# Optimization experiments

Hardware: AMD Instinct MI355X
Metric: run time of the kernel (lower is better)

Reference implementation:

```python
import jax, jax.numpy as jnp
import numpy as np

N = 100000
K = 5
ALPHA = 0.1
IN_DIM, HID_DIM, OUT_DIM = 512, 256, 64


def setup_inputs() -> dict:
    key = jax.random.key(0)
    k1, k2, k3, k4, k5, k6 = jax.random.split(key, 6)
    E = 3200000
    x = jax.random.normal(k1, (N, IN_DIM), dtype=jnp.float32)
    edge_index = jax.random.randint(k2, (2, E), 0, N, dtype=jnp.int32)
    s1 = 1.0 / np.sqrt(IN_DIM)
    s2 = 1.0 / np.sqrt(HID_DIM)
    W1 = jax.random.uniform(k3, (IN_DIM, HID_DIM), jnp.float32, -s1, s1)
    b1 = jax.random.uniform(k4, (HID_DIM,), jnp.float32, -s1, s1)
    W2 = jax.random.uniform(k5, (HID_DIM, OUT_DIM), jnp.float32, -s2, s2)
    b2 = jax.random.uniform(k6, (OUT_DIM,), jnp.float32, -s2, s2)
    return {"x": x, "edge_index": edge_index, "W1": W1, "b1": b1, "W2": W2, "b2": b2}


def _gcn_norm(edge_index, num_nodes):
    # add self loops, symmetric normalization D^-1/2 (A+I) D^-1/2
    loop = jnp.arange(num_nodes, dtype=edge_index.dtype)
    row = jnp.concatenate([edge_index[0], loop])
    col = jnp.concatenate([edge_index[1], loop])
    w = jnp.ones(row.shape[0], dtype=jnp.float32)
    deg = jax.ops.segment_sum(w, col, num_segments=num_nodes)
    dinv = jnp.where(deg > 0, jax.lax.rsqrt(deg), 0.0)
    norm = dinv[row] * w * dinv[col]
    return row, col, norm


def reference(x, edge_index, W1, b1, W2, b2):
    # MLP (dropout = identity in eval mode)
    h = jax.nn.relu(x @ W1 + b1) @ W2 + b2  # [N, OUT_DIM]
    row, col, norm = _gcn_norm(edge_index, N)
    x0 = h
    for _ in range(K):
        msg = h[row] * norm[:, None]                    # gather + scale [E+N, OUT_DIM]
        h = jax.ops.segment_sum(msg, col, num_segments=N)  # scatter-add
        h = (1.0 - ALPHA) * h + ALPHA * x0
    return jax.nn.log_softmax(h, axis=1)
```

## Files before the change

### kernel.cpp

```cpp
#include <hip/hip_runtime.h>

#define IN_DIM  512
#define HID_DIM 256
#define OUT_DIM 64
#define KPROP   5
#define ALPHA   0.1f

#define BKT_SHIFT 9
#define PART_EPB  8192

typedef short short8v __attribute__((ext_vector_type(8)));
typedef float f32x4   __attribute__((ext_vector_type(4)));

__device__ __forceinline__ unsigned short f2bf(float f) {
    unsigned u = __builtin_bit_cast(unsigned, f);
    unsigned r = (u + 0x7FFFu + ((u >> 16) & 1u)) >> 16;
    return (unsigned short)r;
}
__device__ __forceinline__ float bflo(unsigned v) { return __builtin_bit_cast(float, v << 16); }
__device__ __forceinline__ float bfhi(unsigned v) { return __builtin_bit_cast(float, v & 0xffff0000u); }

__global__ __launch_bounds__(256) void bucket_count_kernel(const int* __restrict__ ei, int E,
                                                           int* __restrict__ bucketCnt) {
    __shared__ int hist[256];
    int t = threadIdx.x;
    hist[t] = 0;
    __syncthreads();
    int e0 = blockIdx.x * PART_EPB;
#pragma unroll 4
    for (int i = 0; i < PART_EPB / 256; ++i) {
        int e = e0 + i * 256 + t;
        if (e < E) atomicAdd(&hist[ei[E + e] >> BKT_SHIFT], 1);
    }
    __syncthreads();
    if (hist[t] > 0) atomicAdd(&bucketCnt[t], hist[t]);
}

__global__ __launch_bounds__(256) void bucket_scan_kernel(const int* __restrict__ bucketCnt,
                                                          int* __restrict__ bucketBase,
                                                          int* __restrict__ bucketFill,
                                                          int* __restrict__ indptr,
                                                          int E, int N) {
    __shared__ int sm[256];
    int t = threadIdx.x;
    int v = bucketCnt[t];
    sm[t] = v;
    __syncthreads();
    for (int off = 1; off < 256; off <<= 1) {
        int add = 0;
        if (t >= off) add = sm[t - off];
        __syncthreads();
        if (t >= off) sm[t] += add;
        __syncthreads();
    }
    int base = sm[t] - v;
    bucketBase[t] = base;
    bucketFill[t] = base;
    if (t == 0) indptr[N] = E;
}

__global__ __launch_bounds__(256) void partition_kernel(const int* __restrict__ ei, int E,
                                                        int* __restrict__ bucketFill,
                                                        int* __restrict__ packed) {
    __shared__ int hist[256];
    __shared__ int base[256];
    int t = threadIdx.x;
    int e0 = blockIdx.x * PART_EPB;
    hist[t] = 0;
    __syncthreads();
#pragma unroll 4
    for (int i = 0; i < PART_EPB / 256; ++i) {
        int e = e0 + i * 256 + t;
        if (e < E) atomicAdd(&hist[ei[E + e] >> BKT_SHIFT], 1);
    }
    __syncthreads();
    int cnt = hist[t];
    if (cnt > 0) base[t] = atomicAdd(&bucketFill[t], cnt);
    __syncthreads();
#pragma unroll 4
    for (int i = 0; i < PART_EPB / 256; ++i) {
        int e = e0 + i * 256 + t;
        if (e < E) {
            int dst = ei[E + e];
            int src = ei[e];
            int b = dst >> BKT_SHIFT;
            int pos = atomicAdd(&base[b], 1);
            packed[pos] = ((dst & 511) << 17) | src;
        }
    }
}

__global__ __launch_bounds__(256) void fine_kernel(const int* __restrict__ packed,
                                                   const int* __restrict__ bucketBase,
                                                   const int* __restrict__ bucketCnt,
                                                   int* __restrict__ csr_row,
                                                   int* __restrict__ indptr,
                                                   float* __restrict__ dinv, int N) {
    __shared__ int cnt[512];
    __shared__ int pre[512];
    __shared__ int fill[512];
    __shared__ int sm[256];
    int b = blockIdx.x;
    int t = threadIdx.x;
    int d0 = b << BKT_SHIFT;
    int nd = N - d0;
    if (nd > 512) nd = 512;
    cnt[t] = 0; cnt[t + 256] = 0;
    fill[t] = 0; fill[t + 256] = 0;
    __syncthreads();
    int beg = bucketBase[b];
    int end = beg + bucketCnt[b];
    for (int e = beg + t; e < end; e += 256)
        atomicAdd(&cnt[((unsigned)packed[e]) >> 17], 1);
    __syncthreads();
    int c0 = cnt[2 * t], c1 = cnt[2 * t + 1];
    int s = c0 + c1;
    sm[t] = s;
    __syncthreads();
    for (int off = 1; off < 256; off <<= 1) {
        int add = 0;
        if (t >= off) add = sm[t - off];
        __syncthreads();
        if (t >= off) sm[t] += add;
        __syncthreads();
    }
    int ex = sm[t] - s;
    pre[2 * t] = ex;
    pre[2 * t + 1] = ex + c0;
    __syncthreads();
    for (int dl = t; dl < nd; dl += 256) {
        indptr[d0 + dl] = beg + pre[dl];
        dinv[d0 + dl] = rsqrtf((float)(cnt[dl] + 1));
    }
    for (int e = beg + t; e < end; e += 256) {
        unsigned p = (unsigned)packed[e];
        int dl = (int)(p >> 17);
        int src = (int)(p & 0x1FFFFu);
        int pos = beg + pre[dl] + atomicAdd(&fill[dl], 1);
        csr_row[pos] = src;
    }
}

__global__ __launch_bounds__(256) void prep_w1_kernel(const float* __restrict__ W1,
                                                      unsigned short* __restrict__ w1p) {
    int idx = blockIdx.x * 256 + threadIdx.x;
    int q = idx >> 14;
    int rem = idx & 16383;
    int c = rem >> 6, j = rem & 63;
    w1p[idx] = f2bf(W1[(size_t)(q * 64 + j) * HID_DIM + c]);
}

__global__ __launch_bounds__(256) void prep_w2_kernel(const float* __restrict__ W2,
                                                      unsigned short* __restrict__ w2p) {
    int idx = blockIdx.x * 256 + threadIdx.x;
    int c = idx >> 8, k = idx & 255;
    w2p[idx] = f2bf(W2[(size_t)k * OUT_DIM + c]);
}

struct __align__(16) MlpSmem {
    union {
        struct {
            unsigned short xs[64][72];
            unsigned short ws[256][72];
        } p1;
        struct {
            unsigned short hid[64][264];
            unsigned short w2s[32][264];
        } p2;
    };
};

__device__ __forceinline__ float4 ldx1(const float* __restrict__ x, int row0, int N,
                                       int t, int i, int q) {
    int e = t * 4 + i * 1024;
    int r = e >> 6, j = e & 63;
    if (row0 + r < N) return *(const float4*)&x[(size_t)(row0 + r) * IN_DIM + q * 64 + j];
    return make_float4(0.f, 0.f, 0.f, 0.f);
}

__global__ __launch_bounds__(256, 3) void mlp_mfma_kernel(const float* __restrict__ x,
                                                          const unsigned short* __restrict__ w1p,
                                                          const float* __restrict__ b1,
                                                          const unsigned short* __restrict__ w2p,
                                                          const float* __restrict__ b2,
                                                          const float* __restrict__ dinv,
                                                          float* __restrict__ h0,
                                                          unsigned short* __restrict__ hs,
                                                          int N) {
    __shared__ MlpSmem sm;
    int t = threadIdx.x;
    int w = t >> 6, l = t & 63;
    int l15 = l & 15, l4 = l >> 4;
    int wr0 = w * 16;
    int row0 = blockIdx.x * 64;

    f32x4 acc[16];
#pragma unroll
    for (int i = 0; i < 16; ++i) acc[i] = (f32x4){0.f, 0.f, 0.f, 0.f};

    float4 xr0, xr1, xr2, xr3;
    uint4 wv0, wv1, wv2, wv3, wv4, wv5, wv6, wv7;

#define LOADX(q) do { \
        xr0 = ldx1(x, row0, N, t, 0, (q)); \
        xr1 = ldx1(x, row0, N, t, 1, (q)); \
        xr2 = ldx1(x, row0, N, t, 2, (q)); \
        xr3 = ldx1(x, row0, N, t, 3, (q)); \
    } while (0)
#define LOADW(q) do { \
        const unsigned short* _s = w1p + (q) * 16384; \
        wv0 = *(const uint4*)&_s[t * 8 + 0 * 2048]; \
        wv1 = *(const uint4*)&_s[t * 8 + 1 * 2048]; \
        wv2 = *(const uint4*)&_s[t * 8 + 2 * 2048]; \
        wv3 = *(const uint4*)&_s[t * 8 + 3 * 2048]; \
        wv4 = *(const uint4*)&_s[t * 8 + 4 * 2048]; \
        wv5 = *(const uint4*)&_s[t * 8 + 5 * 2048]; \
        wv6 = *(const uint4*)&_s[t * 8 + 6 * 2048]; \
        wv7 = *(const uint4*)&_s[t * 8 + 7 * 2048]; \
    } while (0)
#define STX(i, v) do { \
        int e = t * 4 + (i) * 1024; \
        int r = e >> 6, j = e & 63; \
        unsigned u0 = (unsigned)f2bf((v).x) | ((unsigned)f2bf((v).y) << 16); \
        unsigned u1 = (unsigned)f2bf((v).z) | ((unsigned)f2bf((v).w) << 16); \
        *(uint2*)&sm.p1.xs[r][j] = make_uint2(u0, u1); \
    } while (0)
#define STW(i, v) do { \
        int e = t * 8 + (i) * 2048; \
        int c = e >> 6, j = e & 63; \
        *(uint4*)&sm.p1.ws[c][j] = (v); \
    } while (0)

    LOADX(0);
    LOADW(0);

    for (int q = 0; q < 8; ++q) {
        __syncthreads();
        STX(0, xr0); STX(1, xr1); STX(2, xr2); STX(3, xr3);
        STW(0, wv0); STW(1, wv1); STW(2, wv2); STW(3, wv3);
        STW(4, wv4); STW(5, wv5); STW(6, wv6); STW(7, wv7);
        __syncthreads();
        if (q < 7) {
            LOADX(q + 1);
            LOADW(q + 1);
        }
#pragma unroll
        for (int s = 0; s < 2; ++s) {
            short8v a = *(const short8v*)&sm.p1.xs[wr0 + l15][s * 32 + l4 * 8];
#pragma unroll
            for (int tc = 0; tc < 16; ++tc) {
                short8v b = *(const short8v*)&sm.p1.ws[tc * 16 + l15][s * 32 + l4 * 8];
                acc[tc] = __builtin_amdgcn_mfma_f32_16x16x32_bf16(a, b, acc[tc], 0, 0, 0);
            }
        }
    }
    __syncthreads();

#pragma unroll
    for (int tc = 0; tc < 16; ++tc) {
        float bv = b1[tc * 16 + l15];
#pragma unroll
        for (int i = 0; i < 4; ++i) {
            float v = fmaxf(acc[tc][i] + bv, 0.f);
            sm.p2.hid[wr0 + l4 * 4 + i][tc * 16 + l15] = f2bf(v);
        }
    }

    f32x4 acc2[4];
#pragma unroll
    for (int i = 0; i < 4; ++i) acc2[i] = (f32x4){0.f, 0.f, 0.f, 0.f};

#pragma unroll
    for (int hf = 0; hf < 2; ++hf) {
#pragma unroll
        for (int i = 0; i < 4; ++i) {
            int e = t * 8 + i * 2048;
            int c = e >> 8, k = e & 255;
            *(uint4*)&sm.p2.w2s[c][k] = *(const uint4*)&w2p[hf * 8192 + e];
        }
        __syncthreads();
#pragma unroll
        for (int s = 0; s < 8; ++s) {
            short8v a = *(const short8v*)&sm.p2.hid[wr0 + l15][s * 32 + l4 * 8];
#pragma unroll
            for (int tcl = 0; tcl < 2; ++tcl) {
                short8v b = *(const short8v*)&sm.p2.w2s[tcl * 16 + l15][s * 32 + l4 * 8];
                acc2[hf * 2 + tcl] =
                    __builtin_amdgcn_mfma_f32_16x16x32_bf16(a, b, acc2[hf * 2 + tcl], 0, 0, 0);
            }
        }
        __syncthreads();
    }

#pragma unroll
    for (int i = 0; i < 4; ++i) {
        int row = row0 + wr0 + l4 * 4 + i;
        if (row < N) {
            float dv = dinv[row];
#pragma unroll
            for (int tc = 0; tc < 4; ++tc) {
                float v = acc2[tc][i] + b2[tc * 16 + l15];
                h0[(size_t)row * OUT_DIM + tc * 16 + l15] = v;
                hs[(size_t)row * OUT_DIM + tc * 16 + l15] = f2bf(dv * v);
            }
        }
    }
#undef LOADX
#undef LOADW
#undef STX
#undef STW
}

__global__ __launch_bounds__(256) void prop_bf16_kernel(const unsigned short* __restrict__ hs,
                                                        const float* __restrict__ h0,
                                                        const float* __restrict__ dinv,
                                                        const int* __restrict__ csr_row,
                                                        const int* __restrict__ indptr,
                                                        unsigned short* __restrict__ hs_out,
                                                        float* __restrict__ hfin,
                                                        int last, int N) {
    int node = blockIdx.x * 4 + (threadIdx.x >> 6);
    if (node >= N) return;
    int l = threadIdx.x & 63;
    int half = l >> 5, li = l & 31;
    const unsigned* hs32 = (const unsigned*)hs;
    int beg = indptr[node], end = indptr[node + 1];
    float a0 = 0.f, a1 = 0.f;
    int e = beg;
    if (e + 8 <= end) {
        int r0 = csr_row[e + 0 + half];
        int r1 = csr_row[e + 2 + half];
        int r2 = csr_row[e + 4 + half];
        int r3 = csr_row[e + 6 + half];
        while (true) {
            int eb = (e + 16 <= end) ? (e + 8) : beg;
            int n0 = csr_row[eb + 0 + half];
            int n1 = csr_row[eb + 2 + half];
            int n2 = csr_row[eb + 4 + half];
            int n3 = csr_row[eb + 6 + half];
            unsigned v0 = hs32[(size_t)r0 * 32 + li];
            unsigned v1 = hs32[(size_t)r1 * 32 + li];
            unsigned v2 = hs32[(size_t)r2 * 32 + li];
            unsigned v3 = hs32[(size_t)r3 * 32 + li];
            a0 += bflo(v0); a1 += bfhi(v0);
            a0 += bflo(v1); a1 += bfhi(v1);
            a0 += bflo(v2); a1 += bfhi(v2);
            a0 += bflo(v3); a1 += bfhi(v3);
            e += 8;
            if (e + 8 > end) break;
            r0 = n0; r1 = n1; r2 = n2; r3 = n3;
        }
    }
    for (; e + 2 <= end; e += 2) {
        int r = csr_row[e + half];
        unsigned v = hs32[(size_t)r * 32 + li];
        a0 += bflo(v); a1 += bfhi(v);
    }
    if (e < end && half == 0) {
        int r = csr_row[e];
        unsigned v = hs32[(size_t)r * 32 + li];
        a0 += bflo(v); a1 += bfhi(v);
    }
    a0 += __shfl_xor(a0, 32);
    a1 += __shfl_xor(a1, 32);
    unsigned vs = hs32[(size_t)node * 32 + li];
    a0 += bflo(vs);
    a1 += bfhi(vs);
    float dcn = dinv[node];
    float2 z = *(const float2*)&h0[(size_t)node * 64 + li * 2];
    float o0 = (1.0f - ALPHA) * (dcn * a0) + ALPHA * z.x;
    float o1 = (1.0f - ALPHA) * (dcn * a1) + ALPHA * z.y;
    if (last) {
        float m = fmaxf(o0, o1);
        m = fmaxf(m, __shfl_xor(m, 1));
        m = fmaxf(m, __shfl_xor(m, 2));
        m = fmaxf(m, __shfl_xor(m, 4));
        m = fmaxf(m, __shfl_xor(m, 8));
        m = fmaxf(m, __shfl_xor(m, 16));
        float s = expf(o0 - m) + expf(o1 - m);
        s += __shfl_xor(s, 1);
        s += __shfl_xor(s, 2);
        s += __shfl_xor(s, 4);
        s += __shfl_xor(s, 8);
        s += __shfl_xor(s, 16);
        float lg = logf(s);
        if (half == 0)
            *(float2*)&hfin[(size_t)node * 64 + li * 2] =
                make_float2(o0 - m - lg, o1 - m - lg);
    } else if (half == 0) {
        unsigned p = (unsigned)f2bf(dcn * o0) | ((unsigned)f2bf(dcn * o1) << 16);
        ((unsigned*)hs_out)[(size_t)node * 32 + li] = p;
    }
}

extern "C" void kernel_launch(void* const* d_in, const int* in_sizes, int n_in,
                              void* d_out, int out_size, void* d_ws, size_t ws_size,
                              hipStream_t stream) {
    const float* x  = (const float*)d_in[0];
    const int*   ei = (const int*)d_in[1];
    const float* W1 = (const float*)d_in[2];
    const float* b1 = (const float*)d_in[3];
    const float* W2 = (const float*)d_in[4];
    const float* b2 = (const float*)d_in[5];
    float* out = (float*)d_out;
    int N = in_sizes[0] / IN_DIM;
    int E = in_sizes[1] / 2;
    int nbkt = (N + 511) >> BKT_SHIFT;

    char* ws = (char*)d_ws;
    size_t off = 0;
    auto alloc = [&](size_t bytes) -> void* {
        void* p = ws + off;
        off += (bytes + 255) & ~(size_t)255;
        return p;
    };
    float* h0     = (float*)alloc((size_t)N * OUT_DIM * 4);
    float* dinv   = (float*)alloc((size_t)N * 4);
    int*   indptr = (int*)alloc((size_t)(N + 1) * 4);
    int*   bcnt   = (int*)alloc(256 * 4);
    int*   bbase  = (int*)alloc(256 * 4);
    int*   bfill  = (int*)alloc(256 * 4);
    int*   packed = (int*)alloc((size_t)E * 4);
    int*   csr_row= (int*)alloc((size_t)E * 4);
    unsigned short* w1p = (unsigned short*)alloc((size_t)IN_DIM * HID_DIM * 2);
    unsigned short* w2p = (unsigned short*)alloc((size_t)HID_DIM * OUT_DIM * 2);
    unsigned short* hsA = (unsigned short*)alloc((size_t)N * OUT_DIM * 2);
    unsigned short* hsB = (unsigned short*)alloc((size_t)N * OUT_DIM * 2);
    (void)ws_size; (void)n_in; (void)out_size;

    hipMemsetAsync(bcnt, 0, 256 * 4, stream);

    prep_w1_kernel<<<(IN_DIM * HID_DIM) / 256, 256, 0, stream>>>(W1, w1p);
    prep_w2_kernel<<<(HID_DIM * OUT_DIM) / 256, 256, 0, stream>>>(W2, w2p);

    int pgrid = (E + PART_EPB - 1) / PART_EPB;
    bucket_count_kernel<<<pgrid, 256, 0, stream>>>(ei, E, bcnt);
    bucket_scan_kernel<<<1, 256, 0, stream>>>(bcnt, bbase, bfill, indptr, E, N);
    partition_kernel<<<pgrid, 256, 0, stream>>>(ei, E, bfill, packed);
    fine_kernel<<<nbkt, 256, 0, stream>>>(packed, bbase, bcnt, csr_row, indptr, dinv, N);

    mlp_mfma_kernel<<<(N + 63) / 64, 256, 0, stream>>>(x, w1p, b1, w2p, b2, dinv,
                                                       h0, hsA, N);

    int pb = (N + 3) / 4;
    for (int it = 0; it < KPROP; ++it) {
        const unsigned short* hin = (it % 2 == 0) ? hsA : hsB;
        unsigned short* hout = (it % 2 == 0) ? hsB : hsA;
        int last = (it == KPROP - 1) ? 1 : 0;
        prop_bf16_kernel<<<pb, 256, 0, stream>>>(hin, h0, dinv, csr_row, indptr,
                                                 hout, out, last, N);
    }
}
```

Baseline: 568.7 us.

## Store propagated features in FP8 and gather four edges per wavefront

Switches the intermediate scaled feature buffers from bf16 to fp8 (e4m3) using the hardware packed convert instructions. Each 64-byte row is now read by 16 lanes, so one wavefront gathers four neighbour rows at once, halving gather bytes in the propagation kernel. The cost is reduced numerical precision in the propagation, which may push results past tolerance, plus a few extra cross-lane reductions.

```diff
diff --git a/kernel.cpp b/kernel.cpp
--- a/kernel.cpp
+++ b/kernel.cpp
@@ -11,14 +11,13 @@
 
 typedef short short8v __attribute__((ext_vector_type(8)));
 typedef float f32x4   __attribute__((ext_vector_type(4)));
+typedef float f32x2   __attribute__((ext_vector_type(2)));
 
 __device__ __forceinline__ unsigned short f2bf(float f) {
     unsigned u = __builtin_bit_cast(unsigned, f);
     unsigned r = (u + 0x7FFFu + ((u >> 16) & 1u)) >> 16;
     return (unsigned short)r;
 }
-__device__ __forceinline__ float bflo(unsigned v) { return __builtin_bit_cast(float, v << 16); }
-__device__ __forceinline__ float bfhi(unsigned v) { return __builtin_bit_cast(float, v & 0xffff0000u); }
 
 __global__ __launch_bounds__(256) void bucket_count_kernel(const int* __restrict__ ei, int E,
                                                            int* __restrict__ bucketCnt) {
@@ -185,7 +184,7 @@
                                                           const float* __restrict__ b2,
                                                           const float* __restrict__ dinv,
                                                           float* __restrict__ h0,
-                                                          unsigned short* __restrict__ hs,
+                                                          unsigned char* __restrict__ hs,
                                                           int N) {
     __shared__ MlpSmem sm;
     int t = threadIdx.x;
@@ -301,7 +300,9 @@
             for (int tc = 0; tc < 4; ++tc) {
                 float v = acc2[tc][i] + b2[tc * 16 + l15];
                 h0[(size_t)row * OUT_DIM + tc * 16 + l15] = v;
-                hs[(size_t)row * OUT_DIM + tc * 16 + l15] = f2bf(dv * v);
+                float sv = dv * v;
+                int pk = __builtin_amdgcn_cvt_pk_fp8_f32(sv, sv, 0, false);
+                hs[(size_t)row * OUT_DIM + tc * 16 + l15] = (unsigned char)(pk & 0xFF);
             }
         }
     }
@@ -311,85 +312,90 @@
 #undef STW
 }
 
-__global__ __launch_bounds__(256) void prop_bf16_kernel(const unsigned short* __restrict__ hs,
-                                                        const float* __restrict__ h0,
-                                                        const float* __restrict__ dinv,
-                                                        const int* __restrict__ csr_row,
-                                                        const int* __restrict__ indptr,
-                                                        unsigned short* __restrict__ hs_out,
-                                                        float* __restrict__ hfin,
-                                                        int last, int N) {
+__global__ __launch_bounds__(256) void prop_fp8_kernel(const unsigned char* __restrict__ hs,
+                                                       const float* __restrict__ h0,
+                                                       const float* __restrict__ dinv,
+                                                       const int* __restrict__ csr_row,
+                                                       const int* __restrict__ indptr,
+                                                       unsigned char* __restrict__ hs_out,
+                                                       float* __restrict__ hfin,
+                                                       int last, int N) {
     int node = blockIdx.x * 4 + (threadIdx.x >> 6);
     if (node >= N) return;
     int l = threadIdx.x & 63;
-    int half = l >> 5, li = l & 31;
-    const unsigned* hs32 = (const unsigned*)hs;
+    int q = l >> 4, lf = l & 15;
+    const unsigned* H = (const unsigned*)hs;
     int beg = indptr[node], end = indptr[node + 1];
-    float a0 = 0.f, a1 = 0.f;
+    float a0 = 0.f, a1 = 0.f, a2 = 0.f, a3 = 0.f;
+#define ACCU(u) do { \
+        f32x2 _f01 = __builtin_amdgcn_cvt_pk_f32_fp8((int)(u), false); \
+        f32x2 _f23 = __builtin_amdgcn_cvt_pk_f32_fp8((int)(u), true);  \
+        a0 += _f01[0]; a1 += _f01[1]; a2 += _f23[0]; a3 += _f23[1];    \
+    } while (0)
     int e = beg;
     if (e + 8 <= end) {
-        int r0 = csr_row[e + 0 + half];
-        int r1 = csr_row[e + 2 + half];
-        int r2 = csr_row[e + 4 + half];
-        int r3 = csr_row[e + 6 + half];
+        int r0 = csr_row[e + q];
+        int r1 = csr_row[e + 4 + q];
         while (true) {
             int eb = (e + 16 <= end) ? (e + 8) : beg;
-            int n0 = csr_row[eb + 0 + half];
-            int n1 = csr_row[eb + 2 + half];
-            int n2 = csr_row[eb + 4 + half];
-            int n3 = csr_row[eb + 6 + half];
-            unsigned v0 = hs32[(size_t)r0 * 32 + li];
-            unsigned v1 = hs32[(size_t)r1 * 32 + li];
-            unsigned v2 = hs32[(size_t)r2 * 32 + li];
-            unsigned v3 = hs32[(size_t)r3 * 32 + li];
-            a0 += bflo(v0); a1 += bfhi(v0);
-            a0 += bflo(v1); a1 += bfhi(v1);
-            a0 += bflo(v2); a1 += bfhi(v2);
-            a0 += bflo(v3); a1 += bfhi(v3);
+            int n0 = csr_row[eb + q];
+            int n1 = csr_row[eb + 4 + q];
+            unsigned u0 = H[(size_t)r0 * 16 + lf];
+            unsigned u1 = H[(size_t)r1 * 16 + lf];
+            ACCU(u0);
+            ACCU(u1);
             e += 8;
             if (e + 8 > end) break;
-            r0 = n0; r1 = n1; r2 = n2; r3 = n3;
-        }
-    }
-    for (; e + 2 <= end; e += 2) {
-        int r = csr_row[e + half];
-        unsigned v = hs32[(size_t)r * 32 + li];
-        a0 += bflo(v); a1 += bfhi(v);
-    }
-    if (e < end && half == 0) {
-        int r = csr_row[e];
-        unsigned v = hs32[(size_t)r * 32 + li];
-        a0 += bflo(v); a1 += bfhi(v);
-    }
-    a0 += __shfl_xor(a0, 32);
-    a1 += __shfl_xor(a1, 32);
-    unsigned vs = hs32[(size_t)node * 32 + li];
-    a0 += bflo(vs);
-    a1 += bfhi(vs);
+            r0 = n0; r1 = n1;
+        }
+    }
+    if (e + 4 <= end) {
+        int r = csr_row[e + q];
+        ACCU(H[(size_t)r * 16 + lf]);
+        e += 4;
+    }
+    if (e + q < end) {
+        int r = csr_row[e + q];
+        ACCU(H[(size_t)r * 16 + lf]);
+    }
+    a0 += __shfl_xor(a0, 16); a1 += __shfl_xor(a1, 16);
+    a2 += __shfl_xor(a2, 16); a3 += __shfl_xor(a3, 16);
+    a0 += __shfl_xor(a0, 32); a1 += __shfl_xor(a1, 32);
+    a2 += __shfl_xor(a2, 32); a3 += __shfl_xor(a3, 32);
+    ACCU(H[(size_t)node * 16 + lf]);
+#undef ACCU
     float dcn = dinv[node];
-    float2 z = *(const float2*)&h0[(size_t)node * 64 + li * 2];
-    float o0 = (1.0f - ALPHA) * (dcn * a0) + ALPHA * z.x;
-    float o1 = (1.0f - ALPHA) * (dcn * a1) + ALPHA * z.y;
     if (last) {
-        float m = fmaxf(o0, o1);
+        float4 z = *(const float4*)&h0[(size_t)node * 64 + lf * 4];
+        float o0 = (1.0f - ALPHA) * (dcn * a0) + ALPHA * z.x;
+        float o1 = (1.0f - ALPHA) * (dcn * a1) + ALPHA * z.y;
+        float o2 = (1.0f - ALPHA) * (dcn * a2) + ALPHA * z.z;
+        float o3 = (1.0f - ALPHA) * (dcn * a3) + ALPHA * z.w;
+        float m = fmaxf(fmaxf(o0, o1), fmaxf(o2, o3));
         m = fmaxf(m, __shfl_xor(m, 1));
         m = fmaxf(m, __shfl_xor(m, 2));
         m = fmaxf(m, __shfl_xor(m, 4));
         m = fmaxf(m, __shfl_xor(m, 8));
-        m = fmaxf(m, __shfl_xor(m, 16));
-        float s = expf(o0 - m) + expf(o1 - m);
+        float s = expf(o0 - m) + expf(o1 - m) + expf(o2 - m) + expf(o3 - m);
         s += __shfl_xor(s, 1);
         s += __shfl_xor(s, 2);
         s += __shfl_xor(s, 4);
         s += __shfl_xor(s, 8);
-        s += __shfl_xor(s, 16);
         float lg = logf(s);
-        if (half == 0)
-            *(float2*)&hfin[(size_t)node * 64 + li * 2] =
-                make_float2(o0 - m - lg, o1 - m - lg);
-    } else if (half == 0) {
-        unsigned p = (unsigned)f2bf(dcn * o0) | ((unsigned)f2bf(dcn * o1) << 16);
-        ((unsigned*)hs_out)[(size_t)node * 32 + li] = p;
+        if (q == 0) {
+            float4 o;
+            o.x = o0 - m - lg; o.y = o1 - m - lg; o.z = o2 - m - lg; o.w = o3 - m - lg;
+            *(float4*)&hfin[(size_t)node * 64 + lf * 4] = o;
+        }
+    } else if (q == 0) {
+        float4 z = *(const float4*)&h0[(size_t)node * 64 + lf * 4];
+        float o0 = (1.0f - ALPHA) * (dcn * a0) + ALPHA * z.x;
+        float o1 = (1.0f - ALPHA) * (dcn * a1) + ALPHA * z.y;
+        float o2 = (1.0f - ALPHA) * (dcn * a2) + ALPHA * z.z;
+        float o3 = (1.0f - ALPHA) * (dcn * a3) + ALPHA * z.w;
+        int wpk = __builtin_amdgcn_cvt_pk_fp8_f32(dcn * o0, dcn * o1, 0, false);
+        wpk = __builtin_amdgcn_cvt_pk_fp8_f32(dcn * o2, dcn * o3, wpk, true);
+        ((unsigned*)hs_out)[(size_t)node * 16 + lf] = (unsigned)wpk;
     }
 }
 
@@ -424,8 +430,8 @@
     int*   csr_row= (int*)alloc((size_t)E * 4);
     unsigned short* w1p = (unsigned short*)alloc((size_t)IN_DIM * HID_DIM * 2);
     unsigned short* w2p = (unsigned short*)alloc((size_t)HID_DIM * OUT_DIM * 2);
-    unsigned short* hsA = (unsigned short*)alloc((size_t)N * OUT_DIM * 2);
-    unsigned short* hsB = (unsigned short*)alloc((size_t)N * OUT_DIM * 2);
+    unsigned char* hsA = (unsigned char*)alloc((size_t)N * OUT_DIM);
+    unsigned char* hsB = (unsigned char*)alloc((size_t)N * OUT_DIM);
     (void)ws_size; (void)n_in; (void)out_size;
 
     hipMemsetAsync(bcnt, 0, 256 * 4, stream);
@@ -444,10 +450,10 @@
 
     int pb = (N + 3) / 4;
     for (int it = 0; it < KPROP; ++it) {
-        const unsigned short* hin = (it % 2 == 0) ? hsA : hsB;
-        unsigned short* hout = (it % 2 == 0) ? hsB : hsA;
+        const unsigned char* hin = (it % 2 == 0) ? hsA : hsB;
+        unsigned char* hout = (it % 2 == 0) ? hsB : hsA;
         int last = (it == KPROP - 1) ? 1 : 0;
-        prop_bf16_kernel<<<pb, 256, 0, stream>>>(hin, h0, dinv, csr_row, indptr,
-                                                 hout, out, last, N);
-    }
-}
+        prop_fp8_kernel<<<pb, 256, 0, stream>>>(hin, h0, dinv, csr_row, indptr,
+                                                hout, out, last, N);
+    }
+}
```

Measured after the change: 529.9 us. -6.8%, faster.
